# Kernel optimization log

Hardware: AMD Instinct MI355X
Metric: run time of the kernel (lower is better)

## Reference

```python
import jax, jax.numpy as jnp
import numpy as np

HEADS = 8
LATENT = 256
D_HEAD = LATENT // HEADS
SCALE = D_HEAD ** -0.5


def setup_inputs() -> dict:
    key = jax.random.key(0)
    ks = jax.random.split(key, 16)
    Bsz, N, dim_a, dim_b = 2, 2048, 768, 768
    def lin(k, din, dout):
        k1, k2 = jax.random.split(k)
        lim = 1.0 / np.sqrt(din)
        W = jax.random.uniform(k1, (din, dout), jnp.float32, -lim, lim)
        b = jax.random.uniform(k2, (dout,), jnp.float32, -lim, lim)
        return W, b
    Wq_aa, bq_aa = lin(ks[0], dim_a, LATENT)
    Wk_aa, bk_aa = lin(ks[1], dim_a, LATENT)
    Wv_a, bv_a = lin(ks[2], dim_a, LATENT)
    Wk_ab, bk_ab = lin(ks[3], dim_a, LATENT)
    Wq_bb, bq_bb = lin(ks[4], dim_b, LATENT)
    Wo, bo = lin(ks[5], LATENT, LATENT)
    A = jax.random.normal(ks[6], (Bsz, N, dim_a), jnp.float32)
    B = jax.random.normal(ks[7], (Bsz, N, dim_b), jnp.float32)
    return dict(A=A, B=B, Wq_aa=Wq_aa, bq_aa=bq_aa, Wk_aa=Wk_aa, bk_aa=bk_aa,
                Wv_a=Wv_a, bv_a=bv_a, Wk_ab=Wk_ab, bk_ab=bk_ab,
                Wq_bb=Wq_bb, bq_bb=bq_bb, Wo=Wo, bo=bo)


def _split_heads(x):
    Bsz, N, _ = x.shape
    return x.reshape(Bsz, N, HEADS, D_HEAD).transpose(0, 2, 1, 3)  # [B,H,N,d]


def reference(A, B, Wq_aa, bq_aa, Wk_aa, bk_aa, Wv_a, bv_a,
              Wk_ab, bk_ab, Wq_bb, bq_bb, Wo, bo):
    Bsz, N, _ = B.shape
    V = _split_heads(A @ Wv_a + bv_a)
    Q_self = _split_heads(A @ Wq_aa + bq_aa)
    K_self = _split_heads(A @ Wk_aa + bk_aa)
    Q_cross = _split_heads(A @ Wk_ab + bk_ab)
    K_cross = _split_heads(B @ Wq_bb + bq_bb)
    attn_self = jnp.einsum('bhnd,bhmd->bhnm', Q_self, K_self) * SCALE
    attn_cross = jnp.einsum('bhnd,bhmd->bhnm', Q_cross, K_cross) * SCALE
    attn = jax.nn.softmax(attn_self + attn_cross, axis=-1)
    out = jnp.einsum('bhnm,bhmd->bhnd', attn, V)
    out = out.transpose(0, 2, 1, 3).reshape(Bsz, N, LATENT)
    return out @ Wo + bo
```

## Files before the change

### kernel.cpp

```cpp
#include <hip/hip_runtime.h>
#include <hip/hip_bf16.h>
#include <math.h>

#define SCALE  0.17677669529663687f
#define QSCALE 0.25501817444361255f

#if __has_builtin(__builtin_amdgcn_exp2f)
#define EXP2(x) __builtin_amdgcn_exp2f(x)
#else
#define EXP2(x) exp2f(x)
#endif

typedef __attribute__((ext_vector_type(8))) short bf16x8;
typedef __attribute__((ext_vector_type(4))) float f32x4;
typedef unsigned int u32;
typedef unsigned short u16;

#define MFMA16(a, b, c) __builtin_amdgcn_mfma_f32_16x16x32_bf16(a, b, c, 0, 0, 0)

__device__ inline u32 bf16rne(float x) {
    u32 u = __float_as_uint(x);
    return (u + 0x7FFFu + ((u >> 16) & 1u)) >> 16;
}
__device__ inline float bf16tof(u32 h) { return __uint_as_float(h << 16); }
__device__ inline u32 pkbf2(float a, float b) {
    union { __hip_bfloat162 h; u32 u; } cv;
    cv.h = __float22bfloat162_rn(make_float2(a, b));
    return cv.u;
}
__device__ inline int swzb(int row, int b) { return row * 128 + (b ^ ((row & 7) << 4)); }

typedef __attribute__((address_space(1))) const u32 gu32;
typedef __attribute__((address_space(3))) u32 lu32;
#define GL16(g, l) __builtin_amdgcn_global_load_lds((gu32*)(const void*)(g), (lu32*)(void*)(l), 16, 0, 0)

__global__ __launch_bounds__(256) void conv_w(
    const float* __restrict__ W0, const float* __restrict__ W1,
    const float* __restrict__ W2, const float* __restrict__ W3,
    const float* __restrict__ W4, const float* __restrict__ Wo,
    u16* __restrict__ W5t_hi, u16* __restrict__ W5t_lo,
    u16* __restrict__ Wot_hi, u16* __restrict__ Wot_lo)
{
    const int g = blockIdx.z;
    const float* W; int K; u16 *dh, *dl;
    switch (g) {
        case 0: W = W0; K = 768; dh = W5t_hi;              dl = nullptr;  break;
        case 1: W = W1; K = 768; dh = W5t_hi + 196608;     dl = nullptr;  break;
        case 2: W = W2; K = 768; dh = W5t_hi + 2 * 196608; dl = nullptr;  break;
        case 3: W = W3; K = 768; dh = W5t_hi + 3 * 196608; dl = nullptr;  break;
        case 4: W = W4; K = 768; dh = W5t_hi + 4 * 196608; dl = nullptr;  break;
        default: W = Wo; K = 256; dh = Wot_hi; dl = Wot_lo; break;
    }
    (void)W5t_lo;
    const int k0 = blockIdx.x * 64, n0 = blockIdx.y * 64;
    if (k0 >= K) return;
    __shared__ float T[64][65];
    const int t = threadIdx.x;
    #pragma unroll
    for (int rep = 0; rep < 4; ++rep) {
        int kr = rep * 16 + (t >> 4);
        int nc = (t & 15) * 4;
        float4 f = *(const float4*)&W[(size_t)(k0 + kr) * 256 + n0 + nc];
        T[kr][nc] = f.x; T[kr][nc + 1] = f.y; T[kr][nc + 2] = f.z; T[kr][nc + 3] = f.w;
    }
    __syncthreads();
    #pragma unroll
    for (int rep = 0; rep < 4; ++rep) {
        int idx = rep * 256 + t;
        int n = idx >> 4, kq = (idx & 15) * 4;
        float v0 = T[kq + 0][n], v1 = T[kq + 1][n], v2 = T[kq + 2][n], v3 = T[kq + 3][n];
        u32 h0 = bf16rne(v0), h1 = bf16rne(v1), h2 = bf16rne(v2), h3 = bf16rne(v3);
        ushort4 hv = {(u16)h0, (u16)h1, (u16)h2, (u16)h3};
        size_t o = (size_t)(n0 + n) * K + k0 + kq;
        *(ushort4*)&dh[o] = hv;
        if (dl) {
            ushort4 lv = {(u16)bf16rne(v0 - bf16tof(h0)), (u16)bf16rne(v1 - bf16tof(h1)),
                          (u16)bf16rne(v2 - bf16tof(h2)), (u16)bf16rne(v3 - bf16tof(h3))};
            *(ushort4*)&dl[o] = lv;
        }
    }
}

__global__ __launch_bounds__(256, 3) void proj_fused(
    const float* __restrict__ A, const float* __restrict__ Bm,
    const u16* __restrict__ W5t_hi,
    const float* __restrict__ b0, const float* __restrict__ b1,
    const float* __restrict__ b2, const float* __restrict__ b3,
    const float* __restrict__ b4,
    u16* __restrict__ Qpk_hi, u16* __restrict__ Qpk_lo,
    u16* __restrict__ Kpk_hi, u16* __restrict__ Vt_hi)
{
    __shared__ u16 XH[64 * 64], XL[64 * 64];
    __shared__ u16 WB[2][128 * 64];

    const int t = threadIdx.x, w = t >> 6, l = t & 63;
    const int l15 = l & 15, lg = l >> 4;

    const int i = blockIdx.x;
    const int v = (i & 7) * 80 + (i >> 3);
    const int unit = v % 10;
    const int g = unit >> 1;
    const int half = unit & 1;
    const int bm = (v / 10) * 64;

    const float* X = (g == 4) ? Bm : A;
    const u16* Wh = W5t_hi + (size_t)g * 196608 + (size_t)half * 98304;
    const float* bias;
    switch (g) {
        case 0: bias = b0; break;
        case 1: bias = b1; break;
        case 2: bias = b2; break;
        case 3: bias = b3; break;
        default: bias = b4; break;
    }
    const bool isq = (g == 0 || g == 3);

    const int lr = l >> 3;
    const int wswz = ((l & 7) * 16) ^ ((lr & 7) << 4);
    const u16* whp = Wh + (size_t)lr * 768 + (wswz >> 1);

    const int xr = t >> 2;
    const float* xp = X + (size_t)(bm + xr) * 768 + (t & 3) * 16;
    const int xb0 = swzb(xr, (t & 3) * 32);
    const int xb1 = swzb(xr, (t & 3) * 32 + 16);

    f32x4 acc[8];
    #pragma unroll
    for (int cg = 0; cg < 8; ++cg) acc[cg] = (f32x4){0.f, 0.f, 0.f, 0.f};

    float4 fc0, fc1, fc2, fc3;
    auto load_x = [&]() {
        fc0 = ((const float4*)xp)[0]; fc1 = ((const float4*)xp)[1];
        fc2 = ((const float4*)xp)[2]; fc3 = ((const float4*)xp)[3];
        xp += 64;
    };
    auto convert_x = [&]() {
        float va[16] = {fc0.x, fc0.y, fc0.z, fc0.w, fc1.x, fc1.y, fc1.z, fc1.w,
                        fc2.x, fc2.y, fc2.z, fc2.w, fc3.x, fc3.y, fc3.z, fc3.w};
        u32 hp[8], lp[8];
        #pragma unroll
        for (int jj = 0; jj < 8; ++jj) {
            float a = va[2 * jj], bq = va[2 * jj + 1];
            u32 hq = pkbf2(a, bq);
            hp[jj] = hq;
            lp[jj] = pkbf2(a - bf16tof(hq & 0xffffu), bq - bf16tof(hq >> 16));
        }
        uint4 u;
        u.x = hp[0]; u.y = hp[1]; u.z = hp[2]; u.w = hp[3];
        *(uint4*)((char*)XH + xb0) = u;
        u.x = hp[4]; u.y = hp[5]; u.z = hp[6]; u.w = hp[7];
        *(uint4*)((char*)XH + xb1) = u;
        u.x = lp[0]; u.y = lp[1]; u.z = lp[2]; u.w = lp[3];
        *(uint4*)((char*)XL + xb0) = u;
        u.x = lp[4]; u.y = lp[5]; u.z = lp[6]; u.w = lp[7];
        *(uint4*)((char*)XL + xb1) = u;
    };
    auto stage_w = [&](u16* buf) {
        #pragma unroll
        for (int j = 0; j < 4; ++j) {
            int c = w * 4 + j;
            GL16(whp + (size_t)c * 6144, &buf[c * 512]);
        }
        whp += 64;
    };

    load_x();
    stage_w(WB[0]);
    convert_x();
    load_x();

    for (int ks = 0; ks < 12; ++ks) {
        __syncthreads();
        if (ks < 11) stage_w(WB[(ks + 1) & 1]);

        const char* Wc = (const char*)WB[ks & 1];
        #pragma unroll
        for (int s = 0; s < 2; ++s) {
            int byo = s * 64 + lg * 16;
            bf16x8 ah = *(const bf16x8*)((const char*)XH + swzb(w * 16 + l15, byo));
            bf16x8 al = *(const bf16x8*)((const char*)XL + swzb(w * 16 + l15, byo));
            #pragma unroll
            for (int cg = 0; cg < 8; ++cg) {
                bf16x8 bh = *(const bf16x8*)(Wc + swzb(cg * 16 + l15, byo));
                acc[cg] = MFMA16(ah, bh, acc[cg]);
                acc[cg] = MFMA16(al, bh, acc[cg]);
            }
        }

        if (ks < 11) {
            convert_x();
            if (ks < 10) load_x();
        }
    }

    float biasv[8];
    #pragma unroll
    for (int cg = 0; cg < 8; ++cg) biasv[cg] = bias[half * 128 + cg * 16 + l15];

    if (g != 2) {
        u16* Dh = isq ? Qpk_hi : Kpk_hi;
        const int dofs = (g == 3 || g == 4) ? 32 : 0;
        #pragma unroll
        for (int cg = 0; cg < 8; ++cg) {
            int c = half * 128 + cg * 16 + l15;
            int h = c >> 5, d = (c & 31) + dofs;
            #pragma unroll
            for (int r = 0; r < 4; ++r) {
                int row = bm + w * 16 + lg * 4 + r;
                float y = acc[cg][r] + biasv[cg];
                if (isq) y *= QSCALE;
                u32 hb = bf16rne(y);
                size_t o = ((size_t)row * 8 + h) * 64 + d;
                Dh[o] = (u16)hb;
                if (isq) Qpk_lo[o] = (u16)bf16rne(y - bf16tof(hb));
            }
        }
    } else {
        __syncthreads();
        #pragma unroll
        for (int cg = 0; cg < 8; ++cg) {
            int dl = cg * 16 + l15;
            #pragma unroll
            for (int r = 0; r < 4; ++r) {
                int kl = w * 16 + lg * 4 + r;
                float y = acc[cg][r] + biasv[cg];
                int byo = (2 * kl) ^ ((dl & 7) << 4);
                *(u16*)((char*)WB[0] + dl * 128 + byo) = (u16)bf16rne(y);
            }
        }
        __syncthreads();
        const int bb = bm >> 11, kb = bm & 2047;
        #pragma unroll
        for (int rep = 0; rep < 8; ++rep) {
            int idx = rep * 256 + t;
            int dl = idx >> 4;
            int kq = idx & 15;
            int dg = half * 128 + dl;
            int h = dg >> 5, d = dg & 31;
            int byo = (8 * kq) ^ ((dl & 7) << 4);
            ushort4 hv = *(const ushort4*)((const char*)WB[0] + dl * 128 + byo);
            size_t o = (((size_t)bb * 8 + h) * 32 + d) * 2048 + kb + kq * 4;
            *(ushort4*)&Vt_hi[o] = hv;
        }
    }
}

__global__ __launch_bounds__(256, 4) void attn_mfma8(
    const u16* __restrict__ Qpk_hi, const u16* __restrict__ Qpk_lo,
    const u16* __restrict__ Kpk_hi, const u16* __restrict__ Vt_hi,
    float* __restrict__ Opart, float* __restrict__ Oml)
{
    __shared__ u16 KH[2][64 * 64], VH[2][32 * 64];
    __shared__ u16 PH[4][16 * 64];

    const int t = threadIdx.x, w = t >> 6, l = t & 63;
    const int l15 = l & 15, lg = l >> 4;

    const int i = blockIdx.x;
    const int v = (i & 7) * 128 + (i >> 3);
    const int panel = v >> 5;
    const int qb   = v & 31;
    const int h = panel >> 2;
    const int z = panel & 3;
    const int b = z >> 1, ks = z & 1;
    const int q0 = qb * 64 + w * 16;
    const int base = b * 2048;

    bf16x8 qh[2], ql[2];
    {
        size_t ro = ((size_t)(base + q0 + l15) * 8 + h) * 64;
        #pragma unroll
        for (int s = 0; s < 2; ++s) {
            qh[s] = *(const bf16x8*)&Qpk_hi[ro + s * 32 + lg * 8];
            ql[s] = *(const bf16x8*)&Qpk_lo[ro + s * 32 + lg * 8];
        }
    }

    const u16* sp[3]; int sstep[3];
    u16* dp0[3]; u16* dp1[3];
    {
        const int k00 = ks * 1024;
        #pragma unroll
        for (int i2 = 0; i2 < 3; ++i2) {
            int c = w + i2 * 4;
            if (c < 8) {
                int r0 = c * 8, r = r0 + (l >> 3);
                int swz = ((l & 7) * 16) ^ ((r & 7) << 4);
                sp[i2] = Kpk_hi + ((size_t)(base + k00 + r) * 8 + h) * 64 + (swz >> 1);
                sstep[i2] = 32768;
                dp0[i2] = &KH[0][r0 * 64];
                dp1[i2] = &KH[1][r0 * 64];
            } else {
                int r0 = (c - 8) * 8, r = r0 + (l >> 3);
                int swz = ((l & 7) * 16) ^ ((r & 7) << 4);
                sp[i2] = Vt_hi + (((size_t)b * 8 + h) * 32 + r) * 2048 + k00 + (swz >> 1);
                sstep[i2] = 64;
                dp0[i2] = &VH[0][r0 * 64];
                dp1[i2] = &VH[1][r0 * 64];
            }
        }
    }

    auto stage = [&](u16* const (&dpx)[3]) {
        #pragma unroll
        for (int i2 = 0; i2 < 3; ++i2) { GL16(sp[i2], dpx[i2]); sp[i2] += sstep[i2]; }
    };

    float m_i = -INFINITY, l_i = 0.f;
    f32x4 o0 = {0.f, 0.f, 0.f, 0.f}, o1 = {0.f, 0.f, 0.f, 0.f};

    auto compute_tile = [&](const u16* KHc, const u16* VHc) {
        f32x4 ta[4] = {{0.f,0.f,0.f,0.f},{0.f,0.f,0.f,0.f},{0.f,0.f,0.f,0.f},{0.f,0.f,0.f,0.f}};
        __builtin_amdgcn_s_setprio(1);
        #pragma unroll
        for (int s = 0; s < 2; ++s) {
            int byo = s * 64 + lg * 16;
            #pragma unroll
            for (int cj = 0; cj < 4; ++cj) {
                bf16x8 kh = *(const bf16x8*)((const char*)KHc + swzb(cj * 16 + l15, byo));
                ta[cj] = MFMA16(kh, qh[s], ta[cj]);
                ta[cj] = MFMA16(kh, ql[s], ta[cj]);
            }
        }
        __builtin_amdgcn_s_setprio(0);

        float t0 = fmaxf(fmaxf(ta[0][0], ta[0][1]), fmaxf(ta[0][2], ta[0][3]));
        float t1 = fmaxf(fmaxf(ta[1][0], ta[1][1]), fmaxf(ta[1][2], ta[1][3]));
        float t2 = fmaxf(fmaxf(ta[2][0], ta[2][1]), fmaxf(ta[2][2], ta[2][3]));
        float t3 = fmaxf(fmaxf(ta[3][0], ta[3][1]), fmaxf(ta[3][2], ta[3][3]));
        float tmax = fmaxf(fmaxf(t0, t1), fmaxf(t2, t3));
        tmax = fmaxf(tmax, __shfl_xor(tmax, 16));
        tmax = fmaxf(tmax, __shfl_xor(tmax, 32));
        if (!__all(tmax <= m_i + 8.0f)) {
            float mnew = fmaxf(m_i, tmax);
            float sc = EXP2(m_i - mnew);
            l_i *= sc;
            #pragma unroll
            for (int r = 0; r < 4; ++r) {
                float fac = __shfl(sc, lg * 4 + r);
                o0[r] *= fac;
                o1[r] *= fac;
            }
            m_i = mnew;
        }
        #pragma unroll
        for (int cj = 0; cj < 4; ++cj)
            #pragma unroll
            for (int r = 0; r < 4; ++r)
                ta[cj][r] = EXP2(ta[cj][r] - m_i);
        float s0 = (ta[0][0] + ta[0][1]) + (ta[0][2] + ta[0][3]);
        float s1 = (ta[1][0] + ta[1][1]) + (ta[1][2] + ta[1][3]);
        float s2 = (ta[2][0] + ta[2][1]) + (ta[2][2] + ta[2][3]);
        float s3 = (ta[3][0] + ta[3][1]) + (ta[3][2] + ta[3][3]);
        float tsum = (s0 + s1) + (s2 + s3);
        tsum += __shfl_xor(tsum, 16);
        tsum += __shfl_xor(tsum, 32);
        l_i += tsum;

        #pragma unroll
        for (int cj = 0; cj < 4; ++cj) {
            uint2 pv = {pkbf2(ta[cj][0], ta[cj][1]), pkbf2(ta[cj][2], ta[cj][3])};
            *(uint2*)((char*)PH[w] + swzb(l15, cj * 32 + lg * 8)) = pv;
        }

        __builtin_amdgcn_s_setprio(1);
        #pragma unroll
        for (int kq = 0; kq < 2; ++kq) {
            int byo = kq * 64 + lg * 16;
            bf16x8 pa  = *(const bf16x8*)((const char*)PH[w] + swzb(l15, byo));
            bf16x8 vh0 = *(const bf16x8*)((const char*)VHc + swzb(l15, byo));
            bf16x8 vh1 = *(const bf16x8*)((const char*)VHc + swzb(16 + l15, byo));
            o0 = MFMA16(pa, vh0, o0);
            o1 = MFMA16(pa, vh1, o1);
        }
        __builtin_amdgcn_s_setprio(0);
    };

    stage(dp0);
    #pragma unroll 1
    for (int it2 = 0; it2 < 8; ++it2) {
        __syncthreads();
        stage(dp1);
        compute_tile(KH[0], VH[0]);
        __syncthreads();
        if (it2 < 7) stage(dp0);
        compute_tile(KH[1], VH[1]);
    }

    const int pb = (b * 8 + h) * 2 + ks;
    #pragma unroll
    for (int r = 0; r < 4; ++r) {
        int row = q0 + lg * 4 + r;
        size_t ob = ((size_t)pb * 2048 + row) * 32;
        Opart[ob + l15]      = o0[r];
        Opart[ob + 16 + l15] = o1[r];
    }
    if (l < 16) {
        int row = q0 + l15;
        float2 ml = {m_i, l_i};
        *(float2*)&Oml[((size_t)pb * 2048 + row) * 2] = ml;
    }
}

__global__ __launch_bounds__(256, 2) void gemm_out_fused(
    const float* __restrict__ Opart, const float* __restrict__ Oml,
    const u16* __restrict__ Wth, const u16* __restrict__ Wtl,
    const float* __restrict__ bias, float* __restrict__ out)
{
    __shared__ u16 XH[64 * 64], XL[64 * 64];
    __shared__ u16 WHB[2][64 * 64], WLB[2][64 * 64];

    const int t = threadIdx.x, w = t >> 6, l = t & 63;
    const int l15 = l & 15, lg = l >> 4;
    const int bn = blockIdx.x * 64, bm = blockIdx.y * 64;
    const int bb = bm >> 11;

    const int lr = l >> 3;
    const int wswz = ((l & 7) * 16) ^ ((lr & 7) << 4);
    const u16* whp = Wth + (size_t)(bn + lr) * 256 + (wswz >> 1);
    const u16* wlp = Wtl + (size_t)(bn + lr) * 256 + (wswz >> 1);

    const int xr = t >> 2;
    const int grl = (bm & 2047) + xr;
    const int hloc = (t >> 1) & 1;
    const int d0 = (t & 1) * 16;
    const int xb0 = swzb(xr, (t & 3) * 32);
    const int xb1 = swzb(xr, (t & 3) * 32 + 16);

    f32x4 acc[4] = {{0.f,0.f,0.f,0.f},{0.f,0.f,0.f,0.f},{0.f,0.f,0.f,0.f},{0.f,0.f,0.f,0.f}};

    float4 op0[4], op1[4];
    float2 ml0, ml1;
    auto load_ctx = [&](int kstep) {
        int hh = kstep * 2 + hloc;
        size_t pb = ((size_t)(bb * 8 + hh)) * 2;
        const float* p0 = &Opart[(pb * 2048 + grl) * 32 + d0];
        const float* p1 = &Opart[((pb + 1) * 2048 + grl) * 32 + d0];
        #pragma unroll
        for (int j = 0; j < 4; ++j) { op0[j] = ((const float4*)p0)[j]; op1[j] = ((const float4*)p1)[j]; }
        ml0 = *(const float2*)&Oml[(pb * 2048 + grl) * 2];
        ml1 = *(const float2*)&Oml[((pb + 1) * 2048 + grl) * 2];
    };
    auto convert_ctx = [&]() {
        float M = fmaxf(ml0.x, ml1.x);
        float w0 = exp2f(ml0.x - M), w1 = exp2f(ml1.x - M);
        float L = ml0.y * w0 + ml1.y * w1;
        float a0 = w0 / L, a1 = w1 / L;
        float y[16];
        #pragma unroll
        for (int j = 0; j < 4; ++j) {
            y[4 * j + 0] = a0 * op0[j].x + a1 * op1[j].x;
            y[4 * j + 1] = a0 * op0[j].y + a1 * op1[j].y;
            y[4 * j + 2] = a0 * op0[j].z + a1 * op1[j].z;
            y[4 * j + 3] = a0 * op0[j].w + a1 * op1[j].w;
        }
        u32 hp[8], lp[8];
        #pragma unroll
        for (int jj = 0; jj < 8; ++jj) {
            float a = y[2 * jj], bq = y[2 * jj + 1];
            u32 hq = pkbf2(a, bq);
            hp[jj] = hq;
            lp[jj] = pkbf2(a - bf16tof(hq & 0xffffu), bq - bf16tof(hq >> 16));
        }
        uint4 u;
        u.x = hp[0]; u.y = hp[1]; u.z = hp[2]; u.w = hp[3];
        *(uint4*)((char*)XH + xb0) = u;
        u.x = hp[4]; u.y = hp[5]; u.z = hp[6]; u.w = hp[7];
        *(uint4*)((char*)XH + xb1) = u;
        u.x = lp[0]; u.y = lp[1]; u.z = lp[2]; u.w = lp[3];
        *(uint4*)((char*)XL + xb0) = u;
        u.x = lp[4]; u.y = lp[5]; u.z = lp[6]; u.w = lp[7];
        *(uint4*)((char*)XL + xb1) = u;
    };
    auto stage_w = [&](int buf) {
        #pragma unroll
        for (int j = 0; j < 4; ++j) {
            int c = w * 4 + j;
            if (c < 8) GL16(whp + (size_t)c * 2048, &WHB[buf][c * 512]);
            else       GL16(wlp + (size_t)(c - 8) * 2048, &WLB[buf][(c - 8) * 512]);
        }
        whp += 64; wlp += 64;
    };

    load_ctx(0);
    stage_w(0);
    convert_ctx();
    load_ctx(1);

    #pragma unroll
    for (int ks = 0; ks < 4; ++ks) {
        __syncthreads();
        if (ks < 3) stage_w((ks + 1) & 1);

        const char* Wh = (const char*)WHB[ks & 1];
        const char* Wl = (const char*)WLB[ks & 1];
        #pragma unroll
        for (int s = 0; s < 2; ++s) {
            int byo = s * 64 + lg * 16;
            bf16x8 ah = *(const bf16x8*)((const char*)XH + swzb(w * 16 + l15, byo));
            bf16x8 al = *(const bf16x8*)((const char*)XL + swzb(w * 16 + l15, byo));
            #pragma unroll
            for (int cj = 0; cj < 4; ++cj) {
                bf16x8 bh = *(const bf16x8*)(Wh + swzb(cj * 16 + l15, byo));
                bf16x8 bl = *(const bf16x8*)(Wl + swzb(cj * 16 + l15, byo));
                acc[cj] = MFMA16(ah, bh, acc[cj]);
                acc[cj] = MFMA16(al, bh, acc[cj]);
                acc[cj] = MFMA16(ah, bl, acc[cj]);
            }
        }

        if (ks < 3) {
            convert_ctx();
            if (ks < 2) load_ctx(ks + 2);
        }
    }

    #pragma unroll
    for (int cj = 0; cj < 4; ++cj) {
        float bv = bias[bn + cj * 16 + l15];
        #pragma unroll
        for (int r = 0; r < 4; ++r) {
            int row = bm + w * 16 + lg * 4 + r;
            out[(size_t)row * 256 + bn + cj * 16 + l15] = acc[cj][r] + bv;
        }
    }
}

extern "C" void kernel_launch(void* const* d_in, const int* in_sizes, int n_in,
                              void* d_out, int out_size, void* d_ws, size_t ws_size,
                              hipStream_t stream) {
    const float* A     = (const float*)d_in[0];
    const float* B     = (const float*)d_in[1];
    const float* Wq_aa = (const float*)d_in[2];
    const float* bq_aa = (const float*)d_in[3];
    const float* Wk_aa = (const float*)d_in[4];
    const float* bk_aa = (const float*)d_in[5];
    const float* Wv_a  = (const float*)d_in[6];
    const float* bv_a  = (const float*)d_in[7];
    const float* Wk_ab = (const float*)d_in[8];
    const float* bk_ab = (const float*)d_in[9];
    const float* Wq_bb = (const float*)d_in[10];
    const float* bq_bb = (const float*)d_in[11];
    const float* Wo    = (const float*)d_in[12];
    const float* bo    = (const float*)d_in[13];
    float* out = (float*)d_out;

    char* p = (char*)d_ws;
    u16* spare0 = (u16*)p; p += 6291456;
    u16* spare1 = (u16*)p; p += 6291456;
    u16* spare2 = (u16*)p; p += 6291456;
    u16* spare3 = (u16*)p; p += 6291456;
    u16* W5t_hi = (u16*)p; p += 1966080;
    u16* W5t_lo = (u16*)p; p += 1966080;
    u16* Wot_hi = (u16*)p; p += 131072;
    u16* Wot_lo = (u16*)p; p += 131072;
    u16* Qpk_hi = (u16*)p; p += 4194304;
    u16* Qpk_lo = (u16*)p; p += 4194304;
    u16* Kpk_hi = (u16*)p; p += 4194304;
    u16* Kpk_lo = (u16*)p; p += 4194304;
    u16* Vt_hi  = (u16*)p; p += 2097152;
    u16* Vt_lo  = (u16*)p; p += 2097152;
    u16* Cx_hi  = (u16*)p; p += 2097152;
    u16* Cx_lo  = (u16*)p; p += 2097152;
    (void)spare0; (void)spare1; (void)spare2; (void)spare3;
    (void)Kpk_lo; (void)Vt_lo; (void)Cx_hi; (void)Cx_lo;

    float* Opart = (float*)d_ws;
    float* Oml   = (float*)((char*)d_ws + 8388608);

    conv_w<<<dim3(12, 4, 6), 256, 0, stream>>>(Wq_aa, Wk_aa, Wv_a, Wk_ab, Wq_bb, Wo,
                                               W5t_hi, W5t_lo, Wot_hi, Wot_lo);
    proj_fused<<<dim3(640), 256, 0, stream>>>(A, B, W5t_hi,
                                              bq_aa, bk_aa, bv_a, bk_ab, bq_bb,
                                              Qpk_hi, Qpk_lo, Kpk_hi, Vt_hi);
    attn_mfma8<<<dim3(1024), 256, 0, stream>>>(Qpk_hi, Qpk_lo, Kpk_hi, Vt_hi,
                                               Opart, Oml);
    gemm_out_fused<<<dim3(4, 64), 256, 0, stream>>>(Opart, Oml, Wot_hi, Wot_lo,
                                                    bo, out);
}
```

Baseline: 80.18 us.

## Triple-buffer K/V tiles in attention with explicit vmcnt waits and barriers

The attention kernel's K/V LDS staging goes from double to triple buffering, so two tiles are in flight while one is computed. The per-tile __syncthreads is replaced by an s_waitcnt vmcnt(3) plus a raw barrier, which waits only for the oldest stage's loads. The s_setprio hints around the MFMA sections are removed and launch bounds drop to 3 blocks per CU to make room for the larger LDS footprint. This hides more global-load latency but costs occupancy, and correctness depends on the hand-written vmcnt count matching the three loads issued per stage.

```diff
diff --git a/kernel.cpp b/kernel.cpp
--- a/kernel.cpp
+++ b/kernel.cpp
@@ -245,12 +245,12 @@
     }
 }
 
-__global__ __launch_bounds__(256, 4) void attn_mfma8(
+__global__ __launch_bounds__(256, 3) void attn_mfma9(
     const u16* __restrict__ Qpk_hi, const u16* __restrict__ Qpk_lo,
     const u16* __restrict__ Kpk_hi, const u16* __restrict__ Vt_hi,
     float* __restrict__ Opart, float* __restrict__ Oml)
 {
-    __shared__ u16 KH[2][64 * 64], VH[2][32 * 64];
+    __shared__ u16 KH[3][64 * 64], VH[3][32 * 64];
     __shared__ u16 PH[4][16 * 64];
 
     const int t = threadIdx.x, w = t >> 6, l = t & 63;
@@ -276,34 +276,33 @@
         }
     }
 
-    const u16* sp[3]; int sstep[3];
-    u16* dp0[3]; u16* dp1[3];
+    const u16* spk0; const u16* spk1; const u16* spv;
+    int koff0, koff1, voff;
     {
         const int k00 = ks * 1024;
-        #pragma unroll
-        for (int i2 = 0; i2 < 3; ++i2) {
-            int c = w + i2 * 4;
-            if (c < 8) {
-                int r0 = c * 8, r = r0 + (l >> 3);
-                int swz = ((l & 7) * 16) ^ ((r & 7) << 4);
-                sp[i2] = Kpk_hi + ((size_t)(base + k00 + r) * 8 + h) * 64 + (swz >> 1);
-                sstep[i2] = 32768;
-                dp0[i2] = &KH[0][r0 * 64];
-                dp1[i2] = &KH[1][r0 * 64];
-            } else {
-                int r0 = (c - 8) * 8, r = r0 + (l >> 3);
-                int swz = ((l & 7) * 16) ^ ((r & 7) << 4);
-                sp[i2] = Vt_hi + (((size_t)b * 8 + h) * 32 + r) * 2048 + k00 + (swz >> 1);
-                sstep[i2] = 64;
-                dp0[i2] = &VH[0][r0 * 64];
-                dp1[i2] = &VH[1][r0 * 64];
-            }
-        }
-    }
-
-    auto stage = [&](u16* const (&dpx)[3]) {
-        #pragma unroll
-        for (int i2 = 0; i2 < 3; ++i2) { GL16(sp[i2], dpx[i2]); sp[i2] += sstep[i2]; }
+        {
+            int r0 = w * 8, r = r0 + (l >> 3);
+            int swz = ((l & 7) * 16) ^ ((r & 7) << 4);
+            spk0 = Kpk_hi + ((size_t)(base + k00 + r) * 8 + h) * 64 + (swz >> 1);
+            koff0 = r0 * 64;
+        }
+        {
+            int r0 = (w + 4) * 8, r = r0 + (l >> 3);
+            int swz = ((l & 7) * 16) ^ ((r & 7) << 4);
+            spk1 = Kpk_hi + ((size_t)(base + k00 + r) * 8 + h) * 64 + (swz >> 1);
+            koff1 = r0 * 64;
+        }
+        {
+            int r0 = w * 8, r = r0 + (l >> 3);
+            int swz = ((l & 7) * 16) ^ ((r & 7) << 4);
+            spv = Vt_hi + (((size_t)b * 8 + h) * 32 + r) * 2048 + k00 + (swz >> 1);
+            voff = r0 * 64;
+        }
+    }
+    auto stageK = [&](u16* kbase, u16* vbase) {
+        GL16(spk0, kbase + koff0); spk0 += 32768;
+        GL16(spk1, kbase + koff1); spk1 += 32768;
+        GL16(spv,  vbase + voff);  spv  += 64;
     };
 
     float m_i = -INFINITY, l_i = 0.f;
@@ -311,7 +310,6 @@
 
     auto compute_tile = [&](const u16* KHc, const u16* VHc) {
         f32x4 ta[4] = {{0.f,0.f,0.f,0.f},{0.f,0.f,0.f,0.f},{0.f,0.f,0.f,0.f},{0.f,0.f,0.f,0.f}};
-        __builtin_amdgcn_s_setprio(1);
         #pragma unroll
         for (int s = 0; s < 2; ++s) {
             int byo = s * 64 + lg * 16;
@@ -322,7 +320,6 @@
                 ta[cj] = MFMA16(kh, ql[s], ta[cj]);
             }
         }
-        __builtin_amdgcn_s_setprio(0);
 
         float t0 = fmaxf(fmaxf(ta[0][0], ta[0][1]), fmaxf(ta[0][2], ta[0][3]));
         float t1 = fmaxf(fmaxf(ta[1][0], ta[1][1]), fmaxf(ta[1][2], ta[1][3]));
@@ -363,7 +360,6 @@
             *(uint2*)((char*)PH[w] + swzb(l15, cj * 32 + lg * 8)) = pv;
         }
 
-        __builtin_amdgcn_s_setprio(1);
         #pragma unroll
         for (int kq = 0; kq < 2; ++kq) {
             int byo = kq * 64 + lg * 16;
@@ -373,19 +369,30 @@
             o0 = MFMA16(pa, vh0, o0);
             o1 = MFMA16(pa, vh1, o1);
         }
-        __builtin_amdgcn_s_setprio(0);
-    };
-
-    stage(dp0);
+    };
+
+    stageK(KH[0], VH[0]);
+    stageK(KH[1], VH[1]);
     #pragma unroll 1
-    for (int it2 = 0; it2 < 8; ++it2) {
-        __syncthreads();
-        stage(dp1);
+    for (int j = 0; j < 5; ++j) {
+        asm volatile("s_waitcnt vmcnt(3) lgkmcnt(0)" ::: "memory");
+        __builtin_amdgcn_s_barrier();
+        if (3 * j + 0 < 14) stageK(KH[2], VH[2]);
         compute_tile(KH[0], VH[0]);
-        __syncthreads();
-        if (it2 < 7) stage(dp0);
+
+        asm volatile("s_waitcnt vmcnt(3) lgkmcnt(0)" ::: "memory");
+        __builtin_amdgcn_s_barrier();
+        if (3 * j + 1 < 14) stageK(KH[0], VH[0]);
         compute_tile(KH[1], VH[1]);
-    }
+
+        asm volatile("s_waitcnt vmcnt(3) lgkmcnt(0)" ::: "memory");
+        __builtin_amdgcn_s_barrier();
+        if (3 * j + 2 < 14) stageK(KH[1], VH[1]);
+        compute_tile(KH[2], VH[2]);
+    }
+    asm volatile("s_waitcnt vmcnt(0) lgkmcnt(0)" ::: "memory");
+    __builtin_amdgcn_s_barrier();
+    compute_tile(KH[0], VH[0]);
 
     const int pb = (b * 8 + h) * 2 + ks;
     #pragma unroll
@@ -573,7 +580,7 @@
     proj_fused<<<dim3(640), 256, 0, stream>>>(A, B, W5t_hi,
                                               bq_aa, bk_aa, bv_a, bk_ab, bq_bb,
                                               Qpk_hi, Qpk_lo, Kpk_hi, Vt_hi);
-    attn_mfma8<<<dim3(1024), 256, 0, stream>>>(Qpk_hi, Qpk_lo, Kpk_hi, Vt_hi,
+    attn_mfma9<<<dim3(1024), 256, 0, stream>>>(Qpk_hi, Qpk_lo, Kpk_hi, Vt_hi,
                                                Opart, Oml);
     gemm_out_fused<<<dim3(4, 64), 256, 0, stream>>>(Opart, Oml, Wot_hi, Wot_lo,
                                                     bo, out);
```

Measured after the change: 84.67 us. 1.06x slower.
